# Optimization experiments

Measured on AMD Instinct MI355X. Metric: run time of the kernel, lower is better.

The kernel has to match this reference:

```python
import jax, jax.numpy as jnp
import numpy as np

B, S, D, H = 8, 2048, 1024, 128  # batch, seq (== CONTEXT_WINDOW), embed dim, headspace


def setup_inputs() -> dict:
    key = jax.random.key(0)
    ks = jax.random.split(key, 7)
    scale = 1.0 / np.sqrt(D)
    return {
        "x": jax.random.normal(ks[0], (B, S, D), dtype=jnp.float32),
        "Wq": jax.random.normal(ks[1], (D, H), dtype=jnp.float32) * scale,
        "bq": jax.random.normal(ks[2], (H,), dtype=jnp.float32) * 0.01,
        "Wk": jax.random.normal(ks[3], (D, H), dtype=jnp.float32) * scale,
        "bk": jax.random.normal(ks[4], (H,), dtype=jnp.float32) * 0.01,
        "Wv": jax.random.normal(ks[5], (D, H), dtype=jnp.float32) * scale,
        "bv": jax.random.normal(ks[6], (H,), dtype=jnp.float32) * 0.01,
    }


def reference(x, Wq, bq, Wk, bk, Wv, bv):
    # x: [B, S, D]
    embedlen = x.shape[-1]
    q = x @ Wq + bq  # [B, S, H]
    k = x @ Wk + bk  # [B, S, H]
    v = x @ Wv + bv  # [B, S, H]
    # NOTE: original code MULTIPLIES by sqrt(embedlen) (embedlen = full embed dim) --
    # faithful reproduction of the source, not the standard 1/sqrt(head_dim).
    scale = jnp.sqrt(jnp.asarray(embedlen, dtype=x.dtype))
    scores = jnp.einsum("bsh,bth->bst", q, k) * scale  # [B, S, S]
    seqlen = x.shape[1]
    causal = jnp.tril(jnp.ones((seqlen, seqlen), dtype=bool))
    scores = jnp.where(causal, scores, -jnp.inf)
    attn = jax.nn.softmax(scores, axis=-1)
    return jnp.einsum("bst,bth->bsh", attn, v)  # [B, S, H]
```

## Files before the change

### kernel.cpp

```cpp
#include <hip/hip_runtime.h>
#include <math.h>

#define SEQ 2048
#define DIM 1024
#define HD  128
#define NB  8
#define M_TOT (NB * SEQ)

typedef __attribute__((ext_vector_type(8))) short   short8;
typedef __attribute__((ext_vector_type(4))) float   floatx4;

__device__ __forceinline__ unsigned short f2bf(float f) {
    unsigned u = __builtin_bit_cast(unsigned, f);
    u += 0x7FFFu + ((u >> 16) & 1u);
    return (unsigned short)(u >> 16);
}
__device__ __forceinline__ float bf2f(unsigned short h) {
    unsigned u = ((unsigned)h) << 16;
    return __builtin_bit_cast(float, u);
}
__device__ __forceinline__ void async16(const void* g, void* l) {
    __builtin_amdgcn_global_load_lds(
        (const __attribute__((address_space(1))) unsigned int*)g,
        (__attribute__((address_space(3))) unsigned int*)l, 16, 0, 0);
}

#define MFMA16(a, b, c) __builtin_amdgcn_mfma_f32_16x16x32_bf16((a), (b), (c), 0, 0, 0)

__global__ __launch_bounds__(256) void wt_prep(
    const float* __restrict__ Wq, const float* __restrict__ Wk, const float* __restrict__ Wv,
    unsigned short* __restrict__ Wth, unsigned short* __restrict__ Wtl)
{
    int idx = blockIdx.x * 256 + threadIdx.x;
    int k   = idx & 1023;
    int n   = (idx >> 10) & 127;
    int mat = idx >> 17;
    const float* W = (mat == 0) ? Wq : (mat == 1) ? Wk : Wv;
    float v = W[k * HD + n];
    unsigned short hi = f2bf(v);
    Wth[idx] = hi;
    Wtl[idx] = f2bf(v - bf2f(hi));
}

__global__ __launch_bounds__(256) void qkv_gemm(
    const float* __restrict__ x,
    const unsigned short* __restrict__ Wth, const unsigned short* __restrict__ Wtl,
    const float* __restrict__ bq, const float* __restrict__ bk, const float* __restrict__ bv,
    unsigned short* __restrict__ Qh, unsigned short* __restrict__ Ql,
    unsigned short* __restrict__ Kh, unsigned short* __restrict__ Kl,
    unsigned short* __restrict__ Vt)
{
    __shared__ short lds[48 * 512];

    const int t    = threadIdx.x;
    const int lane = t & 63;
    const int w    = t >> 6;
    const int lrow = lane & 15;
    const int quad = lane >> 4;

    const int mat = blockIdx.x;
    const int R0  = blockIdx.y * 64;
    const int mh  = w & 1;
    const int nh  = w >> 1;

    floatx4 acc[2][4];
    const floatx4 zf = {0.f, 0.f, 0.f, 0.f};
    #pragma unroll
    for (int i = 0; i < 2; ++i)
        #pragma unroll
        for (int j = 0; j < 4; ++j) acc[i][j] = zf;

    const size_t wmat = (size_t)mat * (HD * DIM);

    auto stage = [&](int k0, int q) {
        #pragma unroll
        for (int i = 0; i < 6; ++i) {
            int id = w * 6 + i;
            const void* src;
            if (id < 8) {
                int mf = id >> 1, c = id & 1;
                src = x + (size_t)(R0 + mf * 16 + lrow) * DIM + k0 + quad * 8 + c * 4;
            } else {
                int bid = id - 8, p = bid & 1, nf = bid >> 1;
                src = (p ? Wtl : Wth) + wmat
                    + (size_t)(nf * 16 + lrow) * DIM + k0 + quad * 8;
            }
            async16(src, &lds[(q * 24 + id) * 512 + lane * 8]);
        }
    };

    stage(0, 0);
    for (int it = 0; it < 32; ++it) {
        __syncthreads();
        if (it < 31) stage((it + 1) * 32, (it + 1) & 1);
        const int q = it & 1;

        short8 ah[2], al[2];
        #pragma unroll
        for (int mi = 0; mi < 2; ++mi) {
            int mf = 2 * mh + mi;
            const float* f0 = (const float*)&lds[(q * 24 + mf * 2 + 0) * 512];
            const float* f1 = (const float*)&lds[(q * 24 + mf * 2 + 1) * 512];
            float4 fa = *(const float4*)&f0[lane * 4];
            float4 fb = *(const float4*)&f1[lane * 4];
            float xv[8] = {fa.x, fa.y, fa.z, fa.w, fb.x, fb.y, fb.z, fb.w};
            #pragma unroll
            for (int i = 0; i < 8; ++i) {
                unsigned short h = f2bf(xv[i]);
                ah[mi][i] = (short)h;
                al[mi][i] = (short)f2bf(xv[i] - bf2f(h));
            }
        }
        #pragma unroll
        for (int ni = 0; ni < 4; ++ni) {
            int nf = nh * 4 + ni;
            short8 bh = *(short8*)&lds[(q * 24 + 8 + nf * 2 + 0) * 512 + lane * 8];
            #pragma unroll
            for (int mi = 0; mi < 2; ++mi)
                acc[mi][ni] = MFMA16(ah[mi], bh, acc[mi][ni]);
            if (mat < 2) {
                short8 bl = *(short8*)&lds[(q * 24 + 8 + nf * 2 + 1) * 512 + lane * 8];
                #pragma unroll
                for (int mi = 0; mi < 2; ++mi) {
                    acc[mi][ni] = MFMA16(ah[mi], bl, acc[mi][ni]);
                    acc[mi][ni] = MFMA16(al[mi], bh, acc[mi][ni]);
                }
            }
        }
    }

    const float* bias = (mat == 0) ? bq : (mat == 1) ? bk : bv;
    #pragma unroll
    for (int ni = 0; ni < 4; ++ni) {
        int col = (nh * 4 + ni) * 16 + lrow;
        float bval = bias[col];
        #pragma unroll
        for (int mi = 0; mi < 2; ++mi) {
            #pragma unroll
            for (int reg = 0; reg < 4; ++reg) {
                int gm = R0 + (2 * mh + mi) * 16 + quad * 4 + reg;
                float v = acc[mi][ni][reg] + bval;
                if (mat == 0) {
                    v *= 32.0f;
                    unsigned short h = f2bf(v);
                    Qh[(size_t)gm * HD + col] = h;
                    Ql[(size_t)gm * HD + col] = f2bf(v - bf2f(h));
                } else if (mat == 1) {
                    unsigned short h = f2bf(v);
                    Kh[(size_t)gm * HD + col] = h;
                    Kl[(size_t)gm * HD + col] = f2bf(v - bf2f(h));
                } else {
                    int b = gm >> 11, s = gm & 2047;
                    Vt[((size_t)b * HD + col) * SEQ + s] = f2bf(v);
                }
            }
        }
    }
}

__global__ __launch_bounds__(256) void flash_attn(
    const unsigned short* __restrict__ Qh, const unsigned short* __restrict__ Ql,
    const unsigned short* __restrict__ Kh, const unsigned short* __restrict__ Kl,
    const unsigned short* __restrict__ Vt, float* __restrict__ out,
    float* __restrict__ Opart, float* __restrict__ ML, int split)
{
    __shared__ short lds[52 * 512];

    const int t    = threadIdx.x;
    const int lane = t & 63;
    const int w    = t >> 6;
    const int lrow = lane & 15;
    const int quad = lane >> 4;

    const int idx = blockIdx.x;
    const int b   = idx & 7;
    const int h   = split ? ((idx >> 3) & 1) : 0;
    const int s   = split ? (31 - (idx >> 4)) : (31 - (idx >> 3));
    const int t0  = split ? (h * (s + 1)) : 0;
    const int t1  = t0 + (split ? (s + 1) : (2 * (s + 1)));

    const int R = s * 64 + w * 16;

    const size_t kbase = (size_t)b * SEQ * HD;
    const size_t vbase = (size_t)b * HD * SEQ;

    short8 qf[4][2];
    #pragma unroll
    for (int kc = 0; kc < 4; ++kc) {
        size_t off = kbase + (size_t)(R + lrow) * HD + kc * 32 + quad * 8;
        qf[kc][0] = *(const short8*)(Qh + off);
        qf[kc][1] = *(const short8*)(Ql + off);
    }

    const floatx4 zf = {0.f, 0.f, 0.f, 0.f};
    floatx4 accO[8];
    #pragma unroll
    for (int i = 0; i < 8; ++i) accO[i] = zf;
    float m_[4] = {-1e30f, -1e30f, -1e30f, -1e30f};
    float l_[4] = {0.f, 0.f, 0.f, 0.f};

    auto stage = [&](int tile, int q) {
        const int j0 = tile * 32;
        #pragma unroll
        for (int i = 0; i < 6; ++i) {
            int id = w * 6 + i;
            const unsigned short* src;
            if (id < 16) {
                int nt = id >> 3, kc = (id >> 1) & 3, p = id & 1;
                src = (p ? Kl : Kh) + kbase
                    + (size_t)(j0 + nt * 16 + lrow) * HD + kc * 32 + quad * 8;
            } else {
                int df = id - 16;
                src = Vt + vbase + (size_t)(df * 16 + lrow) * SEQ + j0 + quad * 8;
            }
            async16(src, &lds[(q * 24 + id) * 512 + lane * 8]);
        }
    };

    stage(t0, 0);
    for (int it = t0; it < t1; ++it) {
        __syncthreads();
        if (it + 1 < t1) stage(it + 1, (it + 1 - t0) & 1);
        const int q  = (it - t0) & 1;
        const int j0 = it * 32;

        if (j0 <= R + 15) {
            floatx4 S[2] = {zf, zf};
            #pragma unroll
            for (int nt = 0; nt < 2; ++nt) {
                #pragma unroll
                for (int kc = 0; kc < 4; ++kc) {
                    short8 khf = *(short8*)&lds[(q * 24 + nt * 8 + kc * 2 + 0) * 512 + lane * 8];
                    short8 klf = *(short8*)&lds[(q * 24 + nt * 8 + kc * 2 + 1) * 512 + lane * 8];
                    S[nt] = MFMA16(qf[kc][0], khf, S[nt]);
                    S[nt] = MFMA16(qf[kc][0], klf, S[nt]);
                    S[nt] = MFMA16(qf[kc][1], khf, S[nt]);
                }
            }
            if (j0 + 31 > R) {
                #pragma unroll
                for (int nt = 0; nt < 2; ++nt) {
                    int key = j0 + nt * 16 + lrow;
                    #pragma unroll
                    for (int reg = 0; reg < 4; ++reg) {
                        if (key > R + quad * 4 + reg) S[nt][reg] = -INFINITY;
                    }
                }
            }
            float alpha[4];
            #pragma unroll
            for (int reg = 0; reg < 4; ++reg) {
                float mx = fmaxf(S[0][reg], S[1][reg]);
                #pragma unroll
                for (int hh = 1; hh < 16; hh <<= 1) mx = fmaxf(mx, __shfl_xor(mx, hh));
                float mnew = fmaxf(fmaxf(m_[reg], mx), -1e30f);
                alpha[reg] = __expf(m_[reg] - mnew);
                m_[reg] = mnew;
                float p0 = __expf(S[0][reg] - mnew);
                float p1 = __expf(S[1][reg] - mnew);
                S[0][reg] = p0; S[1][reg] = p1;
                float ls = p0 + p1;
                #pragma unroll
                for (int hh = 1; hh < 16; hh <<= 1) ls += __shfl_xor(ls, hh);
                l_[reg] = l_[reg] * alpha[reg] + ls;
            }
            #pragma unroll
            for (int i = 0; i < 8; ++i)
                #pragma unroll
                for (int reg = 0; reg < 4; ++reg) accO[i][reg] *= alpha[reg];

            #pragma unroll
            for (int nt = 0; nt < 2; ++nt) {
                #pragma unroll
                for (int reg = 0; reg < 4; ++reg) {
                    int kloc = nt * 16 + lrow;
                    int jj = kloc & 7, q2 = (kloc >> 3) & 3;
                    int lane2 = (quad * 4 + reg) + (q2 << 4);
                    lds[(48 + w) * 512 + lane2 * 8 + jj] = (short)f2bf(S[nt][reg]);
                }
            }
            short8 pf = *(short8*)&lds[(48 + w) * 512 + lane * 8];
            #pragma unroll
            for (int df = 0; df < 8; ++df) {
                short8 vf = *(short8*)&lds[(q * 24 + 16 + df) * 512 + lane * 8];
                accO[df] = MFMA16(pf, vf, accO[df]);
            }
        }
    }

    if (split) {
        float* op = Opart + (size_t)idx * (64 * 128);
        #pragma unroll
        for (int df = 0; df < 8; ++df) {
            #pragma unroll
            for (int reg = 0; reg < 4; ++reg) {
                int rl = w * 16 + quad * 4 + reg;
                op[rl * 128 + df * 16 + lrow] = accO[df][reg];
            }
        }
        if (lrow == 0) {
            #pragma unroll
            for (int reg = 0; reg < 4; ++reg) {
                int rl = w * 16 + quad * 4 + reg;
                ML[(idx * 64 + rl) * 2 + 0] = m_[reg];
                ML[(idx * 64 + rl) * 2 + 1] = l_[reg];
            }
        }
    } else {
        float inv[4];
        #pragma unroll
        for (int reg = 0; reg < 4; ++reg) inv[reg] = 1.0f / l_[reg];
        #pragma unroll
        for (int df = 0; df < 8; ++df) {
            #pragma unroll
            for (int reg = 0; reg < 4; ++reg) {
                size_t o = ((size_t)(b * SEQ + R + quad * 4 + reg)) * HD + df * 16 + lrow;
                out[o] = accO[df][reg] * inv[reg];
            }
        }
    }
}

__global__ __launch_bounds__(256) void splitk_merge(
    const float* __restrict__ Opart, const float* __restrict__ ML,
    float* __restrict__ out)
{
    int tid = blockIdx.x * 256 + threadIdx.x;
    int row = tid >> 5, c4 = tid & 31;
    int b = row >> 11, r = row & 2047, s = r >> 6, rl = r & 63;
    int i0 = ((31 - s) << 4) + b;
    int i1 = i0 + 8;
    float m0 = ML[(i0 * 64 + rl) * 2], l0 = ML[(i0 * 64 + rl) * 2 + 1];
    float m1 = ML[(i1 * 64 + rl) * 2], l1 = ML[(i1 * 64 + rl) * 2 + 1];
    float M  = fmaxf(m0, m1);
    float w0 = __expf(m0 - M), w1 = __expf(m1 - M);
    float inv = 1.0f / (w0 * l0 + w1 * l1);
    float4 a  = *(const float4*)&Opart[((size_t)i0 * 64 + rl) * 128 + c4 * 4];
    float4 bb = *(const float4*)&Opart[((size_t)i1 * 64 + rl) * 128 + c4 * 4];
    float4 o;
    o.x = (w0 * a.x + w1 * bb.x) * inv;
    o.y = (w0 * a.y + w1 * bb.y) * inv;
    o.z = (w0 * a.z + w1 * bb.z) * inv;
    o.w = (w0 * a.w + w1 * bb.w) * inv;
    *(float4*)&out[(size_t)row * 128 + c4 * 4] = o;
}

extern "C" void kernel_launch(void* const* d_in, const int* in_sizes, int n_in,
                              void* d_out, int out_size, void* d_ws, size_t ws_size,
                              hipStream_t stream) {
    const float* x  = (const float*)d_in[0];
    const float* Wq = (const float*)d_in[1];
    const float* bq = (const float*)d_in[2];
    const float* Wk = (const float*)d_in[3];
    const float* bk = (const float*)d_in[4];
    const float* Wv = (const float*)d_in[5];
    const float* bv = (const float*)d_in[6];
    float* out = (float*)d_out;

    unsigned short* Qh  = (unsigned short*)d_ws;
    unsigned short* Ql  = Qh  + (size_t)M_TOT * HD;
    unsigned short* Kh  = Ql  + (size_t)M_TOT * HD;
    unsigned short* Kl  = Kh  + (size_t)M_TOT * HD;
    unsigned short* Vt  = Kl  + (size_t)M_TOT * HD;
    unsigned short* Wth = Vt  + (size_t)M_TOT * HD;
    unsigned short* Wtl = Wth + (size_t)3 * HD * DIM;
    float* Opart = (float*)(Wtl + (size_t)3 * HD * DIM);
    float* ML    = Opart + (size_t)512 * 64 * 128;

    const size_t need = 22544384ULL + 16777216ULL + 262144ULL;
    const int split = (ws_size >= need) ? 1 : 0;

    wt_prep<<<(3 * HD * DIM) / 256, 256, 0, stream>>>(Wq, Wk, Wv, Wth, Wtl);
    qkv_gemm<<<dim3(3, 256), 256, 0, stream>>>(x, Wth, Wtl, bq, bk, bv, Qh, Ql, Kh, Kl, Vt);
    flash_attn<<<split ? 512 : 256, 256, 0, stream>>>(Qh, Ql, Kh, Kl, Vt, out, Opart, ML, split);
    if (split) splitk_merge<<<2048, 256, 0, stream>>>(Opart, ML, out);
}
```

Measured before the change: 246.0 us.

## Convert x tile to bf16 hi/lo once per block via register prefetch

```diff
diff --git a/kernel.cpp b/kernel.cpp
--- a/kernel.cpp
+++ b/kernel.cpp
@@ -58,8 +58,8 @@
     const int lrow = lane & 15;
     const int quad = lane >> 4;
 
-    const int mat = blockIdx.x;
-    const int R0  = blockIdx.y * 64;
+    const int mat = blockIdx.y;
+    const int R0  = blockIdx.x * 64;
     const int mh  = w & 1;
     const int nh  = w >> 1;
 
@@ -71,59 +71,70 @@
         for (int j = 0; j < 4; ++j) acc[i][j] = zf;
 
     const size_t wmat = (size_t)mat * (HD * DIM);
-
-    auto stage = [&](int k0, int q) {
-        #pragma unroll
-        for (int i = 0; i < 6; ++i) {
-            int id = w * 6 + i;
-            const void* src;
-            if (id < 8) {
-                int mf = id >> 1, c = id & 1;
-                src = x + (size_t)(R0 + mf * 16 + lrow) * DIM + k0 + quad * 8 + c * 4;
-            } else {
-                int bid = id - 8, p = bid & 1, nf = bid >> 1;
-                src = (p ? Wtl : Wth) + wmat
-                    + (size_t)(nf * 16 + lrow) * DIM + k0 + quad * 8;
-            }
-            async16(src, &lds[(q * 24 + id) * 512 + lane * 8]);
-        }
+    const float* xp = x + (size_t)(R0 + w * 16 + lrow) * DIM + quad * 8;
+
+    float4 xa, xb;
+    auto loadX = [&](int k0) {
+        xa = *(const float4*)(xp + k0);
+        xb = *(const float4*)(xp + k0 + 4);
     };
-
-    stage(0, 0);
+    auto writeA = [&](int q) {
+        float xv[8] = {xa.x, xa.y, xa.z, xa.w, xb.x, xb.y, xb.z, xb.w};
+        short8 hv, lv;
+        #pragma unroll
+        for (int i = 0; i < 8; ++i) {
+            unsigned short h = f2bf(xv[i]);
+            hv[i] = (short)h;
+            lv[i] = (short)f2bf(xv[i] - bf2f(h));
+        }
+        *(short8*)&lds[(q * 24 + w * 2 + 0) * 512 + lane * 8] = hv;
+        *(short8*)&lds[(q * 24 + w * 2 + 1) * 512 + lane * 8] = lv;
+    };
+    auto stageB = [&](int k0, int q) {
+        #pragma unroll
+        for (int i = 0; i < 4; ++i) {
+            int id = w * 4 + i;
+            int p = id & 1, nf = id >> 1;
+            const unsigned short* src = (p ? Wtl : Wth) + wmat
+                + (size_t)(nf * 16 + lrow) * DIM + k0 + quad * 8;
+            async16(src, &lds[(q * 24 + 8 + id) * 512 + lane * 8]);
+        }
+    };
+
+    loadX(0);
+    writeA(0);
+    stageB(0, 0);
+    loadX(32);
+
     for (int it = 0; it < 32; ++it) {
         __syncthreads();
-        if (it < 31) stage((it + 1) * 32, (it + 1) & 1);
         const int q = it & 1;
-
-        short8 ah[2], al[2];
-        #pragma unroll
-        for (int mi = 0; mi < 2; ++mi) {
-            int mf = 2 * mh + mi;
-            const float* f0 = (const float*)&lds[(q * 24 + mf * 2 + 0) * 512];
-            const float* f1 = (const float*)&lds[(q * 24 + mf * 2 + 1) * 512];
-            float4 fa = *(const float4*)&f0[lane * 4];
-            float4 fb = *(const float4*)&f1[lane * 4];
-            float xv[8] = {fa.x, fa.y, fa.z, fa.w, fb.x, fb.y, fb.z, fb.w};
-            #pragma unroll
-            for (int i = 0; i < 8; ++i) {
-                unsigned short h = f2bf(xv[i]);
-                ah[mi][i] = (short)h;
-                al[mi][i] = (short)f2bf(xv[i] - bf2f(h));
-            }
-        }
+        if (it + 1 < 32) {
+            writeA(1 - q);
+            stageB((it + 1) * 32, 1 - q);
+            if (it + 2 < 32) loadX((it + 2) * 32);
+        }
+
+        short8 a[2][2];
+        #pragma unroll
+        for (int mi = 0; mi < 2; ++mi)
+            #pragma unroll
+            for (int p = 0; p < 2; ++p)
+                a[mi][p] = *(short8*)&lds[(q * 24 + (2 * mh + mi) * 2 + p) * 512 + lane * 8];
+
         #pragma unroll
         for (int ni = 0; ni < 4; ++ni) {
             int nf = nh * 4 + ni;
             short8 bh = *(short8*)&lds[(q * 24 + 8 + nf * 2 + 0) * 512 + lane * 8];
             #pragma unroll
             for (int mi = 0; mi < 2; ++mi)
-                acc[mi][ni] = MFMA16(ah[mi], bh, acc[mi][ni]);
+                acc[mi][ni] = MFMA16(a[mi][0], bh, acc[mi][ni]);
             if (mat < 2) {
                 short8 bl = *(short8*)&lds[(q * 24 + 8 + nf * 2 + 1) * 512 + lane * 8];
                 #pragma unroll
                 for (int mi = 0; mi < 2; ++mi) {
-                    acc[mi][ni] = MFMA16(ah[mi], bl, acc[mi][ni]);
-                    acc[mi][ni] = MFMA16(al[mi], bh, acc[mi][ni]);
+                    acc[mi][ni] = MFMA16(a[mi][0], bl, acc[mi][ni]);
+                    acc[mi][ni] = MFMA16(a[mi][1], bh, acc[mi][ni]);
                 }
             }
         }
@@ -371,7 +382,7 @@
     const int split = (ws_size >= need) ? 1 : 0;
 
     wt_prep<<<(3 * HD * DIM) / 256, 256, 0, stream>>>(Wq, Wk, Wv, Wth, Wtl);
-    qkv_gemm<<<dim3(3, 256), 256, 0, stream>>>(x, Wth, Wtl, bq, bk, bv, Qh, Ql, Kh, Kl, Vt);
+    qkv_gemm<<<dim3(256, 3), 256, 0, stream>>>(x, Wth, Wtl, bq, bk, bv, Qh, Ql, Kh, Kl, Vt);
     flash_attn<<<split ? 512 : 256, 256, 0, stream>>>(Qh, Ql, Kh, Kl, Vt, out, Opart, ML, split);
     if (split) splitk_merge<<<2048, 256, 0, stream>>>(Opart, ML, out);
 }
```

Result: faster. 241.0 us (-2.0%).
